# Kernel tuning notes

Hardware: AMD Instinct MI355X
Metric: run time of the kernel (lower is better)

Reference implementation:

```python
import jax, jax.numpy as jnp
import numpy as np


def flatten_tri(begin, end, T):
    # maps span (begin, end) with length=end-begin into the flattened triangular chart index
    length = end - begin
    return (T + 1) * T // 2 - (T - length + 2) * (T - length + 1) // 2 + begin


def _normalize(x):
    n = jnp.linalg.norm(x, axis=-1, keepdims=True)
    return x / jnp.maximum(n, 1e-12)


def _compose(x, W1, b1, W2, b2):
    h = jax.nn.relu(x @ W1.T + b1)
    return jax.nn.relu(h @ W2.T + b2)


def _bilinear(l, r, Wb):
    # l, r: [N, B, D] -> [N, B, 1]
    return jnp.einsum('nbi,ij,nbj->nb', l, Wb, r)[..., None]


def setup_inputs() -> dict:
    key = jax.random.key(0)
    ks = jax.random.split(key, 6)
    T, B, D = 32, 64, 768
    return {
        'word_embeddings': jax.random.normal(ks[0], (T, B, D), dtype=jnp.float32),
        'Wl': jax.random.normal(ks[1], (D, D), dtype=jnp.float32) * 0.02,
        'bl': jnp.zeros((D,), dtype=jnp.float32),
        'W1': jax.random.normal(ks[2], (D, 2 * D), dtype=jnp.float32) * 0.02,
        'b1': jnp.zeros((D,), dtype=jnp.float32),
        'W2': jax.random.normal(ks[3], (D, D), dtype=jnp.float32) * 0.02,
        'b2': jnp.zeros((D,), dtype=jnp.float32),
        'Wb': jax.random.normal(ks[4], (D, D), dtype=jnp.float32) * 0.02,
        'root_bias': jax.random.normal(ks[5], (D,), dtype=jnp.float32) * 0.02,
    }


def _diora(word_embeddings, Wl, bl, W1, b1, W2, b2, Wb, root_bias):
    T, B, D = word_embeddings.shape
    tri = T * (T + 1) // 2

    inside_vecs = jnp.zeros((tri, B, D), dtype=word_embeddings.dtype)
    inside_scores = jnp.zeros((tri, B, 1), dtype=word_embeddings.dtype)
    # word_linear: Linear + Tanh, then L2 normalize; fills length-1 cells (first T slots)
    inside_vecs = inside_vecs.at[:T].set(_normalize(jnp.tanh(word_embeddings @ Wl.T + bl)))

    # ---------- inside pass ----------
    for length in range(2, T + 1):
        S = T + 1 - length          # num_spans
        C = length - 1              # num_contexts
        begin = np.arange(S)
        end = begin + length
        j = np.arange(1, C + 1)
        cll = flatten_tri(begin[:, None], begin[:, None] + j[None, :], T).reshape(-1)
        clr = flatten_tri(begin[None, :] + j[:, None], end[None, :], T).T.reshape(-1)
        left = inside_vecs[cll]     # [S*C, B, D]
        right = inside_vecs[clr]
        score = (_bilinear(left, right, Wb) + inside_scores[cll] + inside_scores[clr]).reshape(S, C, B, 1)
        vec = _compose(jnp.concatenate([left, right], axis=-1), W1, b1, W2, b2).reshape(S, C, B, D)
        w = jax.nn.softmax(score, axis=1)
        in_score = jnp.sum(w * score, axis=1)
        in_vec = _normalize(jnp.sum(w * vec, axis=1))
        idx = flatten_tri(begin, end, T)
        inside_scores = inside_scores.at[idx].set(in_score)
        inside_vecs = inside_vecs.at[idx].set(in_vec)

    # ---------- outside pass ----------
    outside_vecs = jnp.zeros((tri, B, D), dtype=word_embeddings.dtype)
    outside_scores = jnp.zeros((tri, B, 1), dtype=word_embeddings.dtype)
    root_idx = tri - 1  # flatten_tri(0, T, T)
    outside_vecs = outside_vecs.at[root_idx].set(jnp.broadcast_to(_normalize(root_bias), (B, D)))

    for length in range(T - 1, 0, -1):
        S = T + 1 - length
        C = T - length
        begin = np.arange(S)
        end = begin + length
        j = np.arange(1, C + 1)           # 1..C
        k = np.arange(C, 0, -1)           # C..1
        clp = (np.tril(flatten_tri(begin[None, :] - j[:, None], end[None, :], T).T, -1)
               + np.triu(flatten_tri(begin[:, None], end[:, None] + k[None, :], T), 0)).reshape(-1)
        cls = (np.tril(flatten_tri(begin[None, :] - j[:, None], begin[None, :], T).T, -1)
               + np.triu(flatten_tri(end[:, None], end[:, None] + k[None, :], T), 0)).reshape(-1)
        parents = outside_vecs[clp]
        sisters = inside_vecs[cls]
        score = (_bilinear(parents, sisters, Wb) + outside_scores[clp] + inside_scores[cls]).reshape(S, C, B, 1)
        vec = _compose(jnp.concatenate([parents, sisters], axis=-1), W1, b1, W2, b2).reshape(S, C, B, D)
        w = jax.nn.softmax(score, axis=1)
        out_score = jnp.sum(w * score, axis=1)
        out_vec = _normalize(jnp.sum(w * vec, axis=1))
        idx = flatten_tri(begin, end, T)
        outside_scores = outside_scores.at[idx].set(out_score)
        outside_vecs = outside_vecs.at[idx].set(out_vec)

    return jnp.concatenate([inside_vecs, outside_vecs, inside_scores, outside_scores], axis=-1)


def reference(word_embeddings, Wl, bl, W1, b1, W2, b2, Wb, root_bias):
    return _diora(word_embeddings, Wl, bl, W1, b1, W2, b2, Wb, root_bias)
```

## Files before the change

kernel.cpp:

```cpp
#include <hip/hip_runtime.h>
#include <hip/hip_bf16.h>


#define TRI 528
#define MAXM 63488

typedef __attribute__((ext_vector_type(8))) short bf16x8;
typedef __attribute__((ext_vector_type(4))) float f32x4;

__device__ __host__ __forceinline__ int lvl_off(int l) {
    int r = 33 - l;
    return 528 - ((r * (r + 1)) >> 1);
}

__device__ __forceinline__ float bf2f(unsigned short u) {
    union { unsigned int i; float f; } v;
    v.i = ((unsigned int)u) << 16;
    return v.f;
}
__device__ __forceinline__ unsigned short f2bf(float f) {
    union { float f; unsigned int i; } v;
    v.f = f;
    unsigned int r = v.i + 0x7fffu + ((v.i >> 16) & 1u);
    return (unsigned short)(r >> 16);
}

__device__ __forceinline__ void gload16(const unsigned short* g, unsigned short* l) {
    __builtin_amdgcn_global_load_lds(
        (const __attribute__((address_space(1))) unsigned int*)g,
        (__attribute__((address_space(3))) unsigned int*)l, 16, 0, 0);
}

__device__ __forceinline__ const bf16x8* frag_ptr(const unsigned short* base,
                                                  int row, int kelem) {
    const int byte = (row * 128 + kelem * 2) ^ ((row & 7) << 4);
    return reinterpret_cast<const bf16x8*>(reinterpret_cast<const char*>(base) + byte);
}

template <int AMODE, int EPI>
__launch_bounds__(256)
__global__ void gemm_k(const unsigned short* __restrict__ Abase,
                       const unsigned short* __restrict__ cinH,
                       const unsigned short* __restrict__ coutH,
                       const unsigned short* __restrict__ Bw,
                       const float* __restrict__ bias,
                       float* __restrict__ outF,
                       unsigned short* __restrict__ outH,
                       int K, int len, int C) {
    __shared__ unsigned short As[64 * 64];
    __shared__ unsigned short Bs[128 * 64];

    const int t = threadIdx.x;
    const int m0 = blockIdx.x << 6;
    const int n0 = blockIdx.y << 7;

    int arow[2], acol[2];
#pragma unroll
    for (int i = 0; i < 2; ++i) {
        const int p = (i << 12) + t * 16;
        const int r = p >> 7;
        arow[i] = r;
        acol[i] = ((p & 127) ^ ((r & 7) << 4)) >> 1;
    }
    int brow[4], bcol[4];
#pragma unroll
    for (int i = 0; i < 4; ++i) {
        const int p = (i << 12) + t * 16;
        const int r = p >> 7;
        brow[i] = r;
        bcol[i] = ((p & 127) ^ ((r & 7) << 4)) >> 1;
    }

    const unsigned short *aL[2], *aR[2];
    if (AMODE == 1 || AMODE == 2) {
        const int p = blockIdx.x;
        const int s = p / C, c = p - s * C;
        int cl, cr;
        if (AMODE == 1) {
            const int j = c + 1;
            cl = lvl_off(j) + s;
            cr = lvl_off(len - j) + s + j;
        } else {
            if (c < s) { cl = lvl_off(len + c + 1) + (s - c - 1); cr = lvl_off(c + 1) + (s - c - 1); }
            else       { cl = lvl_off(len + C - c) + s;           cr = lvl_off(C - c) + (s + len); }
        }
#pragma unroll
        for (int i = 0; i < 2; ++i) {
            const int b = arow[i];
            aL[i] = (AMODE == 1 ? cinH : coutH) + ((size_t)cl * 64 + b) * 768;
            aR[i] = cinH + ((size_t)cr * 64 + b) * 768;
        }
    }

    const int wv = t >> 6, lane = t & 63;
    const int lr = lane & 15, kg = lane >> 4;
    const int wr = (wv >> 1) << 5;
    const int wc = (wv & 1) << 6;

    f32x4 acc[2][4] = {};

    for (int k0 = 0; k0 < K; k0 += 64) {
#pragma unroll
        for (int i = 0; i < 2; ++i) {
            const unsigned short* src;
            if (AMODE == 0) {
                src = Abase + (size_t)(m0 + arow[i]) * K + k0 + acol[i];
            } else {
                src = (k0 < 768 ? aL[i] + k0 : aR[i] + (k0 - 768)) + acol[i];
            }
            gload16(src, &As[(i << 11) + t * 8]);
        }
#pragma unroll
        for (int i = 0; i < 4; ++i) {
            const unsigned short* src = Bw + (size_t)(n0 + brow[i]) * K + k0 + bcol[i];
            gload16(src, &Bs[(i << 11) + t * 8]);
        }
        __syncthreads();

#pragma unroll
        for (int kk = 0; kk < 2; ++kk) {
            const int ke = kk * 32 + kg * 8;
            const bf16x8 a0 = *frag_ptr(As, wr + lr, ke);
            const bf16x8 a1 = *frag_ptr(As, wr + 16 + lr, ke);
            const bf16x8 b0 = *frag_ptr(Bs, wc + lr, ke);
            const bf16x8 b1 = *frag_ptr(Bs, wc + 16 + lr, ke);
            const bf16x8 b2 = *frag_ptr(Bs, wc + 32 + lr, ke);
            const bf16x8 b3 = *frag_ptr(Bs, wc + 48 + lr, ke);
            acc[0][0] = __builtin_amdgcn_mfma_f32_16x16x32_bf16(a0, b0, acc[0][0], 0, 0, 0);
            acc[0][1] = __builtin_amdgcn_mfma_f32_16x16x32_bf16(a0, b1, acc[0][1], 0, 0, 0);
            acc[0][2] = __builtin_amdgcn_mfma_f32_16x16x32_bf16(a0, b2, acc[0][2], 0, 0, 0);
            acc[0][3] = __builtin_amdgcn_mfma_f32_16x16x32_bf16(a0, b3, acc[0][3], 0, 0, 0);
            acc[1][0] = __builtin_amdgcn_mfma_f32_16x16x32_bf16(a1, b0, acc[1][0], 0, 0, 0);
            acc[1][1] = __builtin_amdgcn_mfma_f32_16x16x32_bf16(a1, b1, acc[1][1], 0, 0, 0);
            acc[1][2] = __builtin_amdgcn_mfma_f32_16x16x32_bf16(a1, b2, acc[1][2], 0, 0, 0);
            acc[1][3] = __builtin_amdgcn_mfma_f32_16x16x32_bf16(a1, b3, acc[1][3], 0, 0, 0);
        }
        __syncthreads();
    }

    float bs[4];
    if (EPI != 1) {
#pragma unroll
        for (int fn = 0; fn < 4; ++fn) bs[fn] = bias[n0 + wc + fn * 16 + lr];
    }
#pragma unroll
    for (int fm = 0; fm < 2; ++fm) {
#pragma unroll
        for (int fn = 0; fn < 4; ++fn) {
#pragma unroll
            for (int r = 0; r < 4; ++r) {
                const size_t row = (size_t)(m0 + wr + fm * 16 + (kg << 2) + r) * 768;
                const int col = n0 + wc + fn * 16 + lr;
                float v = acc[fm][fn][r];
                if (EPI == 0) {
                    outH[row + col] = f2bf(fmaxf(v + bs[fn], 0.f));
                } else if (EPI == 1) {
                    outH[row + col] = f2bf(v);
                } else {
                    outF[row + col] = tanhf(v + bs[fn]);
                }
            }
        }
    }
}

template <int OUTSIDE>
__launch_bounds__(256)
__global__ void score_k(const unsigned short* __restrict__ cinH,
                        const unsigned short* __restrict__ coutH,
                        const unsigned short* __restrict__ U,
                        const float* __restrict__ isc, const float* __restrict__ osc,
                        float* __restrict__ raw, int len, int C) {
    const int row = blockIdx.x * 4 + (threadIdx.x >> 6);
    const int lane = threadIdx.x & 63;
    const int p = row >> 6, b = row & 63;
    const int s = p / C, c = p - s * C;
    int cl, cr;
    float sadd;
    const unsigned short* L;
    if (!OUTSIDE) {
        const int j = c + 1;
        cl = lvl_off(j) + s;
        cr = lvl_off(len - j) + s + j;
        L = cinH + ((size_t)cl * 64 + b) * 768;
        sadd = isc[cl * 64 + b] + isc[cr * 64 + b];
    } else {
        if (c < s) { cl = lvl_off(len + c + 1) + (s - c - 1); cr = lvl_off(c + 1) + (s - c - 1); }
        else       { cl = lvl_off(len + C - c) + s;           cr = lvl_off(C - c) + (s + len); }
        L = coutH + ((size_t)cl * 64 + b) * 768;
        sadd = osc[cl * 64 + b] + isc[cr * 64 + b];
    }
    const unsigned short* Uv = U + ((size_t)cr * 64 + b) * 768;
    float d = 0.f;
#pragma unroll
    for (int it = 0; it < 3; ++it) {
        const int i = lane * 4 + it * 256;
        ushort4 lv = *reinterpret_cast<const ushort4*>(&L[i]);
        ushort4 uv = *reinterpret_cast<const ushort4*>(&Uv[i]);
        d += bf2f(lv.x) * bf2f(uv.x) + bf2f(lv.y) * bf2f(uv.y) +
             bf2f(lv.z) * bf2f(uv.z) + bf2f(lv.w) * bf2f(uv.w);
    }
#pragma unroll
    for (int o = 32; o; o >>= 1) d += __shfl_xor(d, o);
    if (lane == 0) raw[row] = d + sadd;
}

__launch_bounds__(256)
__global__ void softmax_k(const float* __restrict__ raw, float* __restrict__ w,
                          float* __restrict__ cscore, int C, int S) {
    const int idx = blockIdx.x * 256 + threadIdx.x;
    if (idx >= S * 64) return;
    const int s = idx >> 6, b = idx & 63;
    float m = -1e30f;
    for (int c = 0; c < C; ++c) m = fmaxf(m, raw[((s * C + c) << 6) + b]);
    float sum = 0.f;
    for (int c = 0; c < C; ++c) sum += expf(raw[((s * C + c) << 6) + b] - m);
    const float inv = 1.f / sum;
    float osum = 0.f;
    for (int c = 0; c < C; ++c) {
        const float x = raw[((s * C + c) << 6) + b];
        const float wv = expf(x - m) * inv;
        w[((s * C + c) << 6) + b] = wv;
        osum += wv * x;
    }
    cscore[idx] = osum;
}

__launch_bounds__(256)
__global__ void reduce_norm_k(const unsigned short* __restrict__ V,
                              const float* __restrict__ w,
                              unsigned short* __restrict__ outvH, int C) {
    __shared__ float red[256];
    const int sb = blockIdx.x;
    const int s = sb >> 6, b = sb & 63;
    const int t = threadIdx.x;
    float a0 = 0.f, a1 = 0.f, a2 = 0.f;
    for (int c = 0; c < C; ++c) {
        const int rowi = ((s * C + c) << 6) + b;
        const float wv = w[rowi];
        const unsigned short* vp = V + (size_t)rowi * 768;
        a0 += wv * bf2f(vp[t]);
        a1 += wv * bf2f(vp[t + 256]);
        a2 += wv * bf2f(vp[t + 512]);
    }
    red[t] = a0 * a0 + a1 * a1 + a2 * a2;
    __syncthreads();
    for (int o = 128; o; o >>= 1) {
        if (t < o) red[t] += red[t + o];
        __syncthreads();
    }
    const float scale = 1.f / fmaxf(sqrtf(red[0]), 1e-12f);
    unsigned short* out = outvH + (size_t)sb * 768;
    out[t] = f2bf(a0 * scale);
    out[t + 256] = f2bf(a1 * scale);
    out[t + 512] = f2bf(a2 * scale);
}

__launch_bounds__(256)
__global__ void norm_rows_k(const float* __restrict__ src,
                            unsigned short* __restrict__ dstH) {
    __shared__ float red[256];
    const float* p = src + (size_t)blockIdx.x * 768;
    const int t = threadIdx.x;
    const float a0 = p[t], a1 = p[t + 256], a2 = p[t + 512];
    red[t] = a0 * a0 + a1 * a1 + a2 * a2;
    __syncthreads();
    for (int o = 128; o; o >>= 1) {
        if (t < o) red[t] += red[t + o];
        __syncthreads();
    }
    const float scale = 1.f / fmaxf(sqrtf(red[0]), 1e-12f);
    unsigned short* d = dstH + (size_t)blockIdx.x * 768;
    d[t] = f2bf(a0 * scale);
    d[t + 256] = f2bf(a1 * scale);
    d[t + 512] = f2bf(a2 * scale);
}

__launch_bounds__(256)
__global__ void root_k(const float* __restrict__ rb,
                       unsigned short* __restrict__ coutH) {
    __shared__ float red[256];
    const int t = threadIdx.x;
    const float a0 = rb[t], a1 = rb[t + 256], a2 = rb[t + 512];
    red[t] = a0 * a0 + a1 * a1 + a2 * a2;
    __syncthreads();
    for (int o = 128; o; o >>= 1) {
        if (t < o) red[t] += red[t + o];
        __syncthreads();
    }
    const float scale = 1.f / fmaxf(sqrtf(red[0]), 1e-12f);
    const unsigned short v0 = f2bf(a0 * scale), v1 = f2bf(a1 * scale),
                         v2 = f2bf(a2 * scale);
    for (int b = 0; b < 64; ++b) {
        unsigned short* o = coutH + ((size_t)(527 * 64 + b)) * 768;
        o[t] = v0; o[t + 256] = v1; o[t + 512] = v2;
    }
}

__launch_bounds__(256)
__global__ void cvt_bf16_k(const float* __restrict__ src,
                           unsigned short* __restrict__ dst, int n) {
    const int i = blockIdx.x * 256 + threadIdx.x;
    if (i < n) dst[i] = f2bf(src[i]);
}

__launch_bounds__(256)
__global__ void assemble_k(const unsigned short* __restrict__ cinH,
                           const unsigned short* __restrict__ coutH,
                           const float* __restrict__ isc, const float* __restrict__ osc,
                           float* __restrict__ out) {
    const int sb = blockIdx.x;
    const int t = threadIdx.x;
    const unsigned short* iv = cinH + (size_t)sb * 768;
    const unsigned short* ov = coutH + (size_t)sb * 768;
    float* o = out + (size_t)sb * 1538;
    o[t] = bf2f(iv[t]); o[t + 256] = bf2f(iv[t + 256]); o[t + 512] = bf2f(iv[t + 512]);
    o[768 + t] = bf2f(ov[t]); o[768 + t + 256] = bf2f(ov[t + 256]);
    o[768 + t + 512] = bf2f(ov[t + 512]);
    if (t == 0) { o[1536] = isc[sb]; o[1537] = osc[sb]; }
}

extern "C" void kernel_launch(void* const* d_in, const int* in_sizes, int n_in,
                              void* d_out, int out_size, void* d_ws, size_t ws_size,
                              hipStream_t stream) {
    const float* emb = (const float*)d_in[0];
    const float* Wl = (const float*)d_in[1];
    const float* bl = (const float*)d_in[2];
    const float* W1 = (const float*)d_in[3];
    const float* b1 = (const float*)d_in[4];
    const float* W2 = (const float*)d_in[5];
    const float* b2 = (const float*)d_in[6];
    const float* Wb = (const float*)d_in[7];
    const float* rb = (const float*)d_in[8];
    float* out = (float*)d_out;

    char* ws = (char*)d_ws;
    size_t off = 0;
    auto alloc = [&](size_t bytes) {
        char* p = ws + off;
        off = (off + bytes + 255) & ~(size_t)255;
        return p;
    };
    unsigned short* cinH = (unsigned short*)alloc((size_t)TRI * 64 * 768 * 2);
    unsigned short* coutH = (unsigned short*)alloc((size_t)TRI * 64 * 768 * 2);
    unsigned short* Uh = (unsigned short*)alloc((size_t)TRI * 64 * 768 * 2);
    unsigned short* Hh = (unsigned short*)alloc((size_t)MAXM * 768 * 2);
    unsigned short* Vh = (unsigned short*)alloc((size_t)MAXM * 768 * 2);
    unsigned short* embH = (unsigned short*)alloc((size_t)2048 * 768 * 2);
    float* chart_is = (float*)alloc((size_t)TRI * 64 * 4);
    float* chart_os = (float*)alloc((size_t)TRI * 64 * 4);
    float* raw = (float*)alloc((size_t)MAXM * 4);
    float* wbuf = (float*)alloc((size_t)MAXM * 4);
    unsigned short* Wlh = (unsigned short*)alloc((size_t)768 * 768 * 2);
    unsigned short* W1h = (unsigned short*)alloc((size_t)768 * 1536 * 2);
    unsigned short* W2h = (unsigned short*)alloc((size_t)768 * 768 * 2);
    unsigned short* Wbh = (unsigned short*)alloc((size_t)768 * 768 * 2);
    float* tmpF = (float*)Hh;

    cvt_bf16_k<<<(768 * 768 + 255) / 256, 256, 0, stream>>>(Wl, Wlh, 768 * 768);
    cvt_bf16_k<<<(768 * 1536 + 255) / 256, 256, 0, stream>>>(W1, W1h, 768 * 1536);
    cvt_bf16_k<<<(768 * 768 + 255) / 256, 256, 0, stream>>>(W2, W2h, 768 * 768);
    cvt_bf16_k<<<(768 * 768 + 255) / 256, 256, 0, stream>>>(Wb, Wbh, 768 * 768);
    cvt_bf16_k<<<(2048 * 768 + 255) / 256, 256, 0, stream>>>(emb, embH, 2048 * 768);
    hipMemsetAsync(chart_is, 0, (size_t)TRI * 64 * 4, stream);
    hipMemsetAsync(chart_os, 0, (size_t)TRI * 64 * 4, stream);

    gemm_k<0, 2><<<dim3(32, 6), 256, 0, stream>>>(
        embH, nullptr, nullptr, Wlh, bl, tmpF, nullptr, 768, 0, 0);
    norm_rows_k<<<2048, 256, 0, stream>>>(tmpF, cinH);
    gemm_k<0, 1><<<dim3(32, 6), 256, 0, stream>>>(
        cinH, nullptr, nullptr, Wbh, nullptr, nullptr, Uh, 768, 0, 0);

    for (int len = 2; len <= 32; ++len) {
        const int S = 33 - len, C = len - 1, M = S * C * 64;
        const size_t lo = (size_t)lvl_off(len);
        score_k<0><<<M / 4, 256, 0, stream>>>(cinH, nullptr, Uh, chart_is, nullptr,
                                              raw, len, C);
        softmax_k<<<(S * 64 + 255) / 256, 256, 0, stream>>>(raw, wbuf,
                                                            chart_is + lo * 64, C, S);
        gemm_k<1, 0><<<dim3(M / 64, 6), 256, 0, stream>>>(
            nullptr, cinH, nullptr, W1h, b1, nullptr, Hh, 1536, len, C);
        gemm_k<0, 0><<<dim3(M / 64, 6), 256, 0, stream>>>(
            Hh, nullptr, nullptr, W2h, b2, nullptr, Vh, 768, 0, 0);
        reduce_norm_k<<<S * 64, 256, 0, stream>>>(Vh, wbuf, cinH + lo * 64 * 768, C);
        gemm_k<0, 1><<<dim3(S, 6), 256, 0, stream>>>(
            cinH + lo * 64 * 768, nullptr, nullptr, Wbh, nullptr, nullptr,
            Uh + lo * 64 * 768, 768, 0, 0);
    }

    root_k<<<1, 256, 0, stream>>>(rb, coutH);
    for (int len = 31; len >= 1; --len) {
        const int S = 33 - len, C = 32 - len, M = S * C * 64;
        const size_t lo = (size_t)lvl_off(len);
        score_k<1><<<M / 4, 256, 0, stream>>>(cinH, coutH, Uh, chart_is, chart_os,
                                              raw, len, C);
        softmax_k<<<(S * 64 + 255) / 256, 256, 0, stream>>>(raw, wbuf,
                                                            chart_os + lo * 64, C, S);
        gemm_k<2, 0><<<dim3(M / 64, 6), 256, 0, stream>>>(
            nullptr, cinH, coutH, W1h, b1, nullptr, Hh, 1536, len, C);
        gemm_k<0, 0><<<dim3(M / 64, 6), 256, 0, stream>>>(
            Hh, nullptr, nullptr, W2h, b2, nullptr, Vh, 768, 0, 0);
        reduce_norm_k<<<S * 64, 256, 0, stream>>>(Vh, wbuf, coutH + lo * 64 * 768, C);
    }

    assemble_k<<<TRI * 64, 256, 0, stream>>>(cinH, coutH, chart_is, chart_os, out);
}
```

Baseline: 8.443 ms.

## Enlarge GEMM tile to 128x128 with 512 threads, fuse score+softmax, vectorize reduce

The GEMM kernel now uses 128-row tiles with 8 waves per block, so each block covers two span/context pairs. This halves the number of re-reads of the weight tiles and adds clamping and row masking for odd pair counts. The score and softmax kernels are merged into one block per (span, batch), which removes a launch and the intermediate raw buffer. reduce_norm is vectorized to ushort4 loads and stores. The changes are independent, and the larger tiles may lower occupancy or leave fewer blocks on small levels.

```diff
diff --git a/kernel.cpp b/kernel.cpp
--- a/kernel.cpp
+++ b/kernel.cpp
@@ -38,7 +38,7 @@
 }
 
 template <int AMODE, int EPI>
-__launch_bounds__(256)
+__launch_bounds__(512)
 __global__ void gemm_k(const unsigned short* __restrict__ Abase,
                        const unsigned short* __restrict__ cinH,
                        const unsigned short* __restrict__ coutH,
@@ -46,47 +46,41 @@
                        const float* __restrict__ bias,
                        float* __restrict__ outF,
                        unsigned short* __restrict__ outH,
-                       int K, int len, int C) {
-    __shared__ unsigned short As[64 * 64];
+                       int K, int len, int C, int Mrows) {
+    __shared__ unsigned short As[128 * 64];
     __shared__ unsigned short Bs[128 * 64];
 
     const int t = threadIdx.x;
-    const int m0 = blockIdx.x << 6;
+    const int m0 = blockIdx.x << 7;
     const int n0 = blockIdx.y << 7;
 
     int arow[2], acol[2];
 #pragma unroll
     for (int i = 0; i < 2; ++i) {
-        const int p = (i << 12) + t * 16;
+        const int p = (i << 13) + t * 16;
         const int r = p >> 7;
         arow[i] = r;
         acol[i] = ((p & 127) ^ ((r & 7) << 4)) >> 1;
     }
-    int brow[4], bcol[4];
-#pragma unroll
-    for (int i = 0; i < 4; ++i) {
-        const int p = (i << 12) + t * 16;
-        const int r = p >> 7;
-        brow[i] = r;
-        bcol[i] = ((p & 127) ^ ((r & 7) << 4)) >> 1;
-    }
 
     const unsigned short *aL[2], *aR[2];
     if (AMODE == 1 || AMODE == 2) {
-        const int p = blockIdx.x;
-        const int s = p / C, c = p - s * C;
-        int cl, cr;
-        if (AMODE == 1) {
-            const int j = c + 1;
-            cl = lvl_off(j) + s;
-            cr = lvl_off(len - j) + s + j;
-        } else {
-            if (c < s) { cl = lvl_off(len + c + 1) + (s - c - 1); cr = lvl_off(c + 1) + (s - c - 1); }
-            else       { cl = lvl_off(len + C - c) + s;           cr = lvl_off(C - c) + (s + len); }
-        }
+        const int pairs = Mrows >> 6;
 #pragma unroll
         for (int i = 0; i < 2; ++i) {
-            const int b = arow[i];
+            int p = 2 * blockIdx.x + (arow[i] >> 6);
+            p = min(p, pairs - 1);
+            const int s = p / C, c = p - s * C;
+            int cl, cr;
+            if (AMODE == 1) {
+                const int j = c + 1;
+                cl = lvl_off(j) + s;
+                cr = lvl_off(len - j) + s + j;
+            } else {
+                if (c < s) { cl = lvl_off(len + c + 1) + (s - c - 1); cr = lvl_off(c + 1) + (s - c - 1); }
+                else       { cl = lvl_off(len + C - c) + s;           cr = lvl_off(C - c) + (s + len); }
+            }
+            const int b = arow[i] & 63;
             aL[i] = (AMODE == 1 ? cinH : coutH) + ((size_t)cl * 64 + b) * 768;
             aR[i] = cinH + ((size_t)cr * 64 + b) * 768;
         }
@@ -94,8 +88,8 @@
 
     const int wv = t >> 6, lane = t & 63;
     const int lr = lane & 15, kg = lane >> 4;
-    const int wr = (wv >> 1) << 5;
-    const int wc = (wv & 1) << 6;
+    const int wrow = (wv >> 1) << 5;
+    const int wcol = (wv & 1) << 6;
 
     f32x4 acc[2][4] = {};
 
@@ -104,28 +98,29 @@
         for (int i = 0; i < 2; ++i) {
             const unsigned short* src;
             if (AMODE == 0) {
-                src = Abase + (size_t)(m0 + arow[i]) * K + k0 + acol[i];
+                const int rsrc = min(m0 + arow[i], Mrows - 1);
+                src = Abase + (size_t)rsrc * K + k0 + acol[i];
             } else {
                 src = (k0 < 768 ? aL[i] + k0 : aR[i] + (k0 - 768)) + acol[i];
             }
-            gload16(src, &As[(i << 11) + t * 8]);
-        }
-#pragma unroll
-        for (int i = 0; i < 4; ++i) {
-            const unsigned short* src = Bw + (size_t)(n0 + brow[i]) * K + k0 + bcol[i];
-            gload16(src, &Bs[(i << 11) + t * 8]);
+            gload16(src, &As[(i << 12) + t * 8]);
+        }
+#pragma unroll
+        for (int i = 0; i < 2; ++i) {
+            const unsigned short* src = Bw + (size_t)(n0 + arow[i]) * K + k0 + acol[i];
+            gload16(src, &Bs[(i << 12) + t * 8]);
         }
         __syncthreads();
 
 #pragma unroll
         for (int kk = 0; kk < 2; ++kk) {
             const int ke = kk * 32 + kg * 8;
-            const bf16x8 a0 = *frag_ptr(As, wr + lr, ke);
-            const bf16x8 a1 = *frag_ptr(As, wr + 16 + lr, ke);
-            const bf16x8 b0 = *frag_ptr(Bs, wc + lr, ke);
-            const bf16x8 b1 = *frag_ptr(Bs, wc + 16 + lr, ke);
-            const bf16x8 b2 = *frag_ptr(Bs, wc + 32 + lr, ke);
-            const bf16x8 b3 = *frag_ptr(Bs, wc + 48 + lr, ke);
+            const bf16x8 a0 = *frag_ptr(As, wrow + lr, ke);
+            const bf16x8 a1 = *frag_ptr(As, wrow + 16 + lr, ke);
+            const bf16x8 b0 = *frag_ptr(Bs, wcol + lr, ke);
+            const bf16x8 b1 = *frag_ptr(Bs, wcol + 16 + lr, ke);
+            const bf16x8 b2 = *frag_ptr(Bs, wcol + 32 + lr, ke);
+            const bf16x8 b3 = *frag_ptr(Bs, wcol + 48 + lr, ke);
             acc[0][0] = __builtin_amdgcn_mfma_f32_16x16x32_bf16(a0, b0, acc[0][0], 0, 0, 0);
             acc[0][1] = __builtin_amdgcn_mfma_f32_16x16x32_bf16(a0, b1, acc[0][1], 0, 0, 0);
             acc[0][2] = __builtin_amdgcn_mfma_f32_16x16x32_bf16(a0, b2, acc[0][2], 0, 0, 0);
@@ -141,7 +136,7 @@
     float bs[4];
     if (EPI != 1) {
 #pragma unroll
-        for (int fn = 0; fn < 4; ++fn) bs[fn] = bias[n0 + wc + fn * 16 + lr];
+        for (int fn = 0; fn < 4; ++fn) bs[fn] = bias[n0 + wcol + fn * 16 + lr];
     }
 #pragma unroll
     for (int fm = 0; fm < 2; ++fm) {
@@ -149,8 +144,10 @@
         for (int fn = 0; fn < 4; ++fn) {
 #pragma unroll
             for (int r = 0; r < 4; ++r) {
-                const size_t row = (size_t)(m0 + wr + fm * 16 + (kg << 2) + r) * 768;
-                const int col = n0 + wc + fn * 16 + lr;
+                const int grow = m0 + wrow + fm * 16 + (kg << 2) + r;
+                if (grow >= Mrows) continue;
+                const size_t row = (size_t)grow * 768;
+                const int col = n0 + wcol + fn * 16 + lr;
                 float v = acc[fm][fn][r];
                 if (EPI == 0) {
                     outH[row + col] = f2bf(fmaxf(v + bs[fn], 0.f));
@@ -166,64 +163,65 @@
 
 template <int OUTSIDE>
 __launch_bounds__(256)
-__global__ void score_k(const unsigned short* __restrict__ cinH,
-                        const unsigned short* __restrict__ coutH,
-                        const unsigned short* __restrict__ U,
-                        const float* __restrict__ isc, const float* __restrict__ osc,
-                        float* __restrict__ raw, int len, int C) {
-    const int row = blockIdx.x * 4 + (threadIdx.x >> 6);
-    const int lane = threadIdx.x & 63;
-    const int p = row >> 6, b = row & 63;
-    const int s = p / C, c = p - s * C;
-    int cl, cr;
-    float sadd;
-    const unsigned short* L;
-    if (!OUTSIDE) {
-        const int j = c + 1;
-        cl = lvl_off(j) + s;
-        cr = lvl_off(len - j) + s + j;
-        L = cinH + ((size_t)cl * 64 + b) * 768;
-        sadd = isc[cl * 64 + b] + isc[cr * 64 + b];
-    } else {
-        if (c < s) { cl = lvl_off(len + c + 1) + (s - c - 1); cr = lvl_off(c + 1) + (s - c - 1); }
-        else       { cl = lvl_off(len + C - c) + s;           cr = lvl_off(C - c) + (s + len); }
-        L = coutH + ((size_t)cl * 64 + b) * 768;
-        sadd = osc[cl * 64 + b] + isc[cr * 64 + b];
-    }
-    const unsigned short* Uv = U + ((size_t)cr * 64 + b) * 768;
-    float d = 0.f;
-#pragma unroll
-    for (int it = 0; it < 3; ++it) {
-        const int i = lane * 4 + it * 256;
-        ushort4 lv = *reinterpret_cast<const ushort4*>(&L[i]);
-        ushort4 uv = *reinterpret_cast<const ushort4*>(&Uv[i]);
-        d += bf2f(lv.x) * bf2f(uv.x) + bf2f(lv.y) * bf2f(uv.y) +
-             bf2f(lv.z) * bf2f(uv.z) + bf2f(lv.w) * bf2f(uv.w);
-    }
-#pragma unroll
-    for (int o = 32; o; o >>= 1) d += __shfl_xor(d, o);
-    if (lane == 0) raw[row] = d + sadd;
-}
-
-__launch_bounds__(256)
-__global__ void softmax_k(const float* __restrict__ raw, float* __restrict__ w,
-                          float* __restrict__ cscore, int C, int S) {
-    const int idx = blockIdx.x * 256 + threadIdx.x;
-    if (idx >= S * 64) return;
-    const int s = idx >> 6, b = idx & 63;
-    float m = -1e30f;
-    for (int c = 0; c < C; ++c) m = fmaxf(m, raw[((s * C + c) << 6) + b]);
-    float sum = 0.f;
-    for (int c = 0; c < C; ++c) sum += expf(raw[((s * C + c) << 6) + b] - m);
-    const float inv = 1.f / sum;
-    float osum = 0.f;
-    for (int c = 0; c < C; ++c) {
-        const float x = raw[((s * C + c) << 6) + b];
-        const float wv = expf(x - m) * inv;
-        w[((s * C + c) << 6) + b] = wv;
-        osum += wv * x;
-    }
-    cscore[idx] = osum;
+__global__ void scoresm_k(const unsigned short* __restrict__ cinH,
+                          const unsigned short* __restrict__ coutH,
+                          const unsigned short* __restrict__ U,
+                          const float* __restrict__ isc, const float* __restrict__ osc,
+                          float* __restrict__ wbuf, float* __restrict__ cscore,
+                          int len, int C) {
+    __shared__ float sc[32];
+    const int s = blockIdx.x >> 6, b = blockIdx.x & 63;
+    const int t = threadIdx.x;
+    const int wv = t >> 6, lane = t & 63;
+
+    for (int c = wv; c < C; c += 4) {
+        int cl, cr;
+        float sadd;
+        const unsigned short* L;
+        if (!OUTSIDE) {
+            const int j = c + 1;
+            cl = lvl_off(j) + s;
+            cr = lvl_off(len - j) + s + j;
+            L = cinH + ((size_t)cl * 64 + b) * 768;
+            sadd = isc[cl * 64 + b] + isc[cr * 64 + b];
+        } else {
+            if (c < s) { cl = lvl_off(len + c + 1) + (s - c - 1); cr = lvl_off(c + 1) + (s - c - 1); }
+            else       { cl = lvl_off(len + C - c) + s;           cr = lvl_off(C - c) + (s + len); }
+            L = coutH + ((size_t)cl * 64 + b) * 768;
+            sadd = osc[cl * 64 + b] + isc[cr * 64 + b];
+        }
+        const unsigned short* Uv = U + ((size_t)cr * 64 + b) * 768;
+        float d = 0.f;
+#pragma unroll
+        for (int it = 0; it < 3; ++it) {
+            const int i = lane * 4 + it * 256;
+            ushort4 lv = *reinterpret_cast<const ushort4*>(&L[i]);
+            ushort4 uv = *reinterpret_cast<const ushort4*>(&Uv[i]);
+            d += bf2f(lv.x) * bf2f(uv.x) + bf2f(lv.y) * bf2f(uv.y) +
+                 bf2f(lv.z) * bf2f(uv.z) + bf2f(lv.w) * bf2f(uv.w);
+        }
+#pragma unroll
+        for (int o = 32; o; o >>= 1) d += __shfl_xor(d, o);
+        if (lane == 0) sc[c] = d + sadd;
+    }
+    __syncthreads();
+
+    if (t < 64) {
+        const float x = (t < C) ? sc[t] : -1e30f;
+        float m = x;
+#pragma unroll
+        for (int o = 32; o; o >>= 1) m = fmaxf(m, __shfl_xor(m, o));
+        const float e = (t < C) ? expf(x - m) : 0.f;
+        float sum = e;
+#pragma unroll
+        for (int o = 32; o; o >>= 1) sum += __shfl_xor(sum, o);
+        const float wv2 = e / sum;
+        float ws = (t < C) ? wv2 * x : 0.f;
+#pragma unroll
+        for (int o = 32; o; o >>= 1) ws += __shfl_xor(ws, o);
+        if (t < C) wbuf[((s * C + t) << 6) + b] = wv2;
+        if (t == 0) cscore[s * 64 + b] = ws;
+    }
 }
 
 __launch_bounds__(256)
@@ -234,26 +232,34 @@
     const int sb = blockIdx.x;
     const int s = sb >> 6, b = sb & 63;
     const int t = threadIdx.x;
-    float a0 = 0.f, a1 = 0.f, a2 = 0.f;
+    float a0 = 0.f, a1 = 0.f, a2 = 0.f, a3 = 0.f;
+    const int e = t * 4;
     for (int c = 0; c < C; ++c) {
         const int rowi = ((s * C + c) << 6) + b;
         const float wv = w[rowi];
-        const unsigned short* vp = V + (size_t)rowi * 768;
-        a0 += wv * bf2f(vp[t]);
-        a1 += wv * bf2f(vp[t + 256]);
-        a2 += wv * bf2f(vp[t + 512]);
-    }
-    red[t] = a0 * a0 + a1 * a1 + a2 * a2;
+        if (t < 192) {
+            ushort4 v = *reinterpret_cast<const ushort4*>(&V[(size_t)rowi * 768 + e]);
+            a0 += wv * bf2f(v.x);
+            a1 += wv * bf2f(v.y);
+            a2 += wv * bf2f(v.z);
+            a3 += wv * bf2f(v.w);
+        }
+    }
+    red[t] = (t < 192) ? (a0 * a0 + a1 * a1 + a2 * a2 + a3 * a3) : 0.f;
     __syncthreads();
     for (int o = 128; o; o >>= 1) {
         if (t < o) red[t] += red[t + o];
         __syncthreads();
     }
     const float scale = 1.f / fmaxf(sqrtf(red[0]), 1e-12f);
-    unsigned short* out = outvH + (size_t)sb * 768;
-    out[t] = f2bf(a0 * scale);
-    out[t + 256] = f2bf(a1 * scale);
-    out[t + 512] = f2bf(a2 * scale);
+    if (t < 192) {
+        ushort4 ov;
+        ov.x = f2bf(a0 * scale);
+        ov.y = f2bf(a1 * scale);
+        ov.z = f2bf(a2 * scale);
+        ov.w = f2bf(a3 * scale);
+        *reinterpret_cast<ushort4*>(&outvH[(size_t)sb * 768 + e]) = ov;
+    }
 }
 
 __launch_bounds__(256)
@@ -349,7 +355,6 @@
     unsigned short* embH = (unsigned short*)alloc((size_t)2048 * 768 * 2);
     float* chart_is = (float*)alloc((size_t)TRI * 64 * 4);
     float* chart_os = (float*)alloc((size_t)TRI * 64 * 4);
-    float* raw = (float*)alloc((size_t)MAXM * 4);
     float* wbuf = (float*)alloc((size_t)MAXM * 4);
     unsigned short* Wlh = (unsigned short*)alloc((size_t)768 * 768 * 2);
     unsigned short* W1h = (unsigned short*)alloc((size_t)768 * 1536 * 2);
@@ -365,41 +370,39 @@
     hipMemsetAsync(chart_is, 0, (size_t)TRI * 64 * 4, stream);
     hipMemsetAsync(chart_os, 0, (size_t)TRI * 64 * 4, stream);
 
-    gemm_k<0, 2><<<dim3(32, 6), 256, 0, stream>>>(
-        embH, nullptr, nullptr, Wlh, bl, tmpF, nullptr, 768, 0, 0);
+    gemm_k<0, 2><<<dim3(16, 6), 512, 0, stream>>>(
+        embH, nullptr, nullptr, Wlh, bl, tmpF, nullptr, 768, 0, 0, 2048);
     norm_rows_k<<<2048, 256, 0, stream>>>(tmpF, cinH);
-    gemm_k<0, 1><<<dim3(32, 6), 256, 0, stream>>>(
-        cinH, nullptr, nullptr, Wbh, nullptr, nullptr, Uh, 768, 0, 0);
+    gemm_k<0, 1><<<dim3(16, 6), 512, 0, stream>>>(
+        cinH, nullptr, nullptr, Wbh, nullptr, nullptr, Uh, 768, 0, 0, 2048);
 
     for (int len = 2; len <= 32; ++len) {
-        const int S = 33 - len, C = len - 1, M = S * C * 64;
+        const int S = 33 - len, C = len - 1;
+        const int pairs = S * C, M = pairs * 64;
         const size_t lo = (size_t)lvl_off(len);
-        score_k<0><<<M / 4, 256, 0, stream>>>(cinH, nullptr, Uh, chart_is, nullptr,
-                                              raw, len, C);
-        softmax_k<<<(S * 64 + 255) / 256, 256, 0, stream>>>(raw, wbuf,
-                                                            chart_is + lo * 64, C, S);
-        gemm_k<1, 0><<<dim3(M / 64, 6), 256, 0, stream>>>(
-            nullptr, cinH, nullptr, W1h, b1, nullptr, Hh, 1536, len, C);
-        gemm_k<0, 0><<<dim3(M / 64, 6), 256, 0, stream>>>(
-            Hh, nullptr, nullptr, W2h, b2, nullptr, Vh, 768, 0, 0);
+        scoresm_k<0><<<S * 64, 256, 0, stream>>>(cinH, nullptr, Uh, chart_is, nullptr,
+                                                 wbuf, chart_is + lo * 64, len, C);
+        gemm_k<1, 0><<<dim3((pairs + 1) / 2, 6), 512, 0, stream>>>(
+            nullptr, cinH, nullptr, W1h, b1, nullptr, Hh, 1536, len, C, M);
+        gemm_k<0, 0><<<dim3((pairs + 1) / 2, 6), 512, 0, stream>>>(
+            Hh, nullptr, nullptr, W2h, b2, nullptr, Vh, 768, 0, 0, M);
         reduce_norm_k<<<S * 64, 256, 0, stream>>>(Vh, wbuf, cinH + lo * 64 * 768, C);
-        gemm_k<0, 1><<<dim3(S, 6), 256, 0, stream>>>(
+        gemm_k<0, 1><<<dim3((S + 1) / 2, 6), 512, 0, stream>>>(
             cinH + lo * 64 * 768, nullptr, nullptr, Wbh, nullptr, nullptr,
-            Uh + lo * 64 * 768, 768, 0, 0);
+            Uh + lo * 64 * 768, 768, 0, 0, S * 64);
     }
 
     root_k<<<1, 256, 0, stream>>>(rb, coutH);
     for (int len = 31; len >= 1; --len) {
-        const int S = 33 - len, C = 32 - len, M = S * C * 64;
+        const int S = 33 - len, C = 32 - len;
+        const int pairs = S * C, M = pairs * 64;
         const size_t lo = (size_t)lvl_off(len);
-        score_k<1><<<M / 4, 256, 0, stream>>>(cinH, coutH, Uh, chart_is, chart_os,
-                                              raw, len, C);
-        softmax_k<<<(S * 64 + 255) / 256, 256, 0, stream>>>(raw, wbuf,
-                                                            chart_os + lo * 64, C, S);
-        gemm_k<2, 0><<<dim3(M / 64, 6), 256, 0, stream>>>(
-            nullptr, cinH, coutH, W1h, b1, nullptr, Hh, 1536, len, C);
-        gemm_k<0, 0><<<dim3(M / 64, 6), 256, 0, stream>>>(
-            Hh, nullptr, nullptr, W2h, b2, nullptr, Vh, 768, 0, 0);
+        scoresm_k<1><<<S * 64, 256, 0, stream>>>(cinH, coutH, Uh, chart_is, chart_os,
+                                                 wbuf, chart_os + lo * 64, len, C);
+        gemm_k<2, 0><<<dim3((pairs + 1) / 2, 6), 512, 0, stream>>>(
+            nullptr, cinH, coutH, W1h, b1, nullptr, Hh, 1536, len, C, M);
+        gemm_k<0, 0><<<dim3((pairs + 1) / 2, 6), 512, 0, stream>>>(
+            Hh, nullptr, nullptr, W2h, b2, nullptr, Vh, 768, 0, 0, M);
         reduce_norm_k<<<S * 64, 256, 0, stream>>>(Vh, wbuf, coutH + lo * 64 * 768, C);
     }
 
```

Result: faster. 8.215 ms (-2.7%).
